# Performance work log

Measured on AMD Instinct MI355X. Metric: run time of the kernel, lower is better.

The kernel has to match this reference:

```python
import jax, jax.numpy as jnp
import numpy as np
from functools import partial

ITERS = 100
EPSILON = 0.8
TAU = 1.02
FEATURE_DIM = 256
MATCHED_THRESHOLD = 0.2
B, D, N0, N1 = 1, 256, 2048, 2048


def log_optimal_transport_extended(scores, alpha, iters, epsilon, tau):
    b, m, n = scores.shape
    dt = scores.dtype
    ms = jnp.asarray(m, dt)
    ns = jnp.asarray(n, dt)
    bins0 = jnp.broadcast_to(alpha, (b, m, 1)).astype(dt)
    bins1 = jnp.broadcast_to(alpha, (b, 1, n)).astype(dt)
    corner = jnp.broadcast_to(alpha, (b, 1, 1)).astype(dt)
    # couplings: [b, m+1, n+1] score matrix augmented with dustbin row/col
    couplings = jnp.concatenate([
        jnp.concatenate([scores, bins0], axis=-1),
        jnp.concatenate([bins1, corner], axis=-1)], axis=1)
    norm = -jnp.log(ms + ns)
    log_mu = jnp.concatenate([jnp.full((m,), norm, dt), (jnp.log(ns) + norm)[None]])
    log_nu = jnp.concatenate([jnp.full((n,), norm, dt), (jnp.log(ms) + norm)[None]])
    log_mu = jnp.broadcast_to(log_mu[None], (b, m + 1))
    log_nu = jnp.broadcast_to(log_nu[None], (b, n + 1))

    def step(carry, _):
        u, v = carry
        u_new = (log_mu - jax.scipy.special.logsumexp(couplings + v[:, None, :], axis=2)) / tau
        u = u + epsilon * (u_new - u)
        v_new = (log_nu - jax.scipy.special.logsumexp(couplings + u[:, :, None], axis=1)) / tau
        v = v + epsilon * (v_new - v)
        return (u, v), None

    u0 = jnp.zeros_like(log_mu)
    v0 = jnp.zeros_like(log_nu)
    (u, v), _ = jax.lax.scan(jax.checkpoint(step), (u0, v0), None, length=iters)
    Z = couplings + u[:, :, None] + v[:, None, :]
    return Z - norm


def reference(mdesc0, mdesc1, bin_score):
    # mdesc0: [b, d, n], mdesc1: [b, d, m]
    sim = jnp.einsum('bdn,bdm->bnm', mdesc0, mdesc1)
    scores = sim / np.float32(np.sqrt(FEATURE_DIM))
    Z = log_optimal_transport_extended(scores, bin_score, ITERS, EPSILON, TAU)
    inner = Z[:, :-1, :-1]                       # [b, m, n]
    m, n = inner.shape[1], inner.shape[2]
    max0_vals = inner.max(axis=2)
    indices0 = inner.argmax(axis=2)              # [b, m] int
    indices1 = inner.argmax(axis=1)              # [b, n] int
    mutual0 = jnp.arange(m)[None, :] == jnp.take_along_axis(indices1, indices0, axis=1)
    mutual1 = jnp.arange(n)[None, :] == jnp.take_along_axis(indices0, indices1, axis=1)
    zero = jnp.zeros((), inner.dtype)
    mscores0 = jnp.where(mutual0, jnp.exp(max0_vals), zero)
    mscores1 = jnp.where(mutual1, jnp.take_along_axis(mscores0, indices1, axis=1), zero)
    valid0 = mutual0 & (mscores0 > MATCHED_THRESHOLD)
    valid1 = mutual1 & jnp.take_along_axis(valid0, indices1, axis=1)
    i0 = jnp.where(valid0, indices0, -1)
    i1 = jnp.where(valid1, indices1, -1)
    return (jnp.exp(Z[0]), i0[0], i1[0], mscores0[0], mscores1[0])


def setup_inputs() -> dict:
    key = jax.random.key(0)
    k0, k1 = jax.random.split(key)
    mdesc0 = jax.random.normal(k0, (B, D, N0), dtype=jnp.float32)
    mdesc1 = jax.random.normal(k1, (B, D, N1), dtype=jnp.float32)
    bin_score = jnp.ones((), dtype=jnp.float32)  # learned dustbin score, init 1.0
    return {"mdesc0": mdesc0, "mdesc1": mdesc1, "bin_score": bin_score}
```

## Files before the change

### kernel.cpp

```cpp
#include <hip/hip_runtime.h>
#include <hip/hip_bf16.h>
#include <math.h>

#define D        256
#define NINNER   2048
#define NROW     2049
#define SP       2064
#define ITERS_N  100
#define EPS_F    0.8f
#define TAU_F    1.02f
#define NB       256
#define NT       256

typedef unsigned long long u64;

#define PSTRIDE  2112u

#define SZ_MAT   (2049u * 2064u)
#define OFF_E    0u
#define OFF_F    SZ_MAT
#define OFF_WUP  (2u * SZ_MAT)
#define OFF_WVP  (OFF_WUP + 4u * PSTRIDE)
#define OFF_MAX0 (OFF_WVP + 4u * PSTRIDE)
#define OFF_IDX0 (OFF_MAX0 + 2048u)
#define OFF_IDX1 (OFF_IDX0 + 2048u)
#define OFF_MS0  (OFF_IDX1 + 2048u)
#define OFF_VLD0 (OFF_MS0 + 2048u)

#define OOFF_Z   0u
#define OOFF_I0  (2049u * 2049u)
#define OOFF_I1  (OOFF_I0 + 2048u)
#define OOFF_S0  (OOFF_I1 + 2048u)
#define OOFF_S1  (OOFF_S0 + 2048u)

__device__ __forceinline__ float    pair_val(u64 x) { return __uint_as_float((unsigned)x); }
__device__ __forceinline__ unsigned pair_tag(u64 x) { return (unsigned)(x >> 32); }
__device__ __forceinline__ u64 make_pair(float v, unsigned t) {
    return ((u64)t << 32) | (u64)__float_as_uint(v);
}

__global__ __launch_bounds__(256) void k_gemm(const float* __restrict__ A,
                                              const float* __restrict__ Bm,
                                              float* __restrict__ E,
                                              float* __restrict__ F) {
    __shared__ float As[8][64];
    __shared__ float Bs[8][64];
    const int tid = threadIdx.x;
    const int tx = tid & 15, ty = tid >> 4;
    const int row0 = blockIdx.y * 64, col0 = blockIdx.x * 64;
    float acc[4][4] = {};
    const int lr = tid >> 6, lc = tid & 63;
    for (int k0 = 0; k0 < D; k0 += 8) {
        As[lr][lc]     = A[(k0 + lr) * NINNER + row0 + lc];
        As[lr + 4][lc] = A[(k0 + lr + 4) * NINNER + row0 + lc];
        Bs[lr][lc]     = Bm[(k0 + lr) * NINNER + col0 + lc];
        Bs[lr + 4][lc] = Bm[(k0 + lr + 4) * NINNER + col0 + lc];
        __syncthreads();
#pragma unroll
        for (int kk = 0; kk < 8; ++kk) {
            const float4 av = *(const float4*)&As[kk][ty * 4];
            const float4 bv = *(const float4*)&Bs[kk][tx * 4];
            const float a_[4] = {av.x, av.y, av.z, av.w};
            const float b_[4] = {bv.x, bv.y, bv.z, bv.w};
#pragma unroll
            for (int r = 0; r < 4; ++r)
#pragma unroll
                for (int c = 0; c < 4; ++c)
                    acc[r][c] = fmaf(a_[r], b_[c], acc[r][c]);
        }
        __syncthreads();
    }
    float o[4][4];
#pragma unroll
    for (int r = 0; r < 4; ++r)
#pragma unroll
        for (int c = 0; c < 4; ++c)
            o[r][c] = expf(acc[r][c] * 0.0625f);
    const int row = row0 + ty * 4, col = col0 + tx * 4;
#pragma unroll
    for (int r = 0; r < 4; ++r)
        *(float4*)(E + (size_t)(row + r) * SP + col)
            = make_float4(o[r][0], o[r][1], o[r][2], o[r][3]);
#pragma unroll
    for (int c = 0; c < 4; ++c)
        *(float4*)(F + (size_t)(col + c) * SP + row)
            = make_float4(o[0][c], o[1][c], o[2][c], o[3][c]);
}

__global__ __launch_bounds__(256) void k_init(float* __restrict__ E,
                                              float* __restrict__ F,
                                              u64* __restrict__ wvb0,
                                              const float* __restrict__ alpha) {
    const int t = blockIdx.x * 256 + threadIdx.x;
    const float ea = expf(alpha[0]);
    if (t < NINNER) {
        E[(size_t)t * SP + NINNER] = ea;
        F[(size_t)t * SP + NINNER] = ea;
    }
    if (t <= NINNER) {
        E[(size_t)NINNER * SP + t] = ea;
        F[(size_t)NINNER * SP + t] = ea;
        wvb0[t] = make_pair(1.0f, 0u);
    }
}

__device__ __forceinline__ void poll8(const u64* buf, int tid, unsigned want, float* w) {
    u64 a[8];
#pragma unroll
    for (int q = 0; q < 8; ++q)
        a[q] = __hip_atomic_load(buf + q * 256 + tid, __ATOMIC_RELAXED, __HIP_MEMORY_SCOPE_AGENT);
    for (;;) {
        unsigned miss = 0u;
#pragma unroll
        for (int q = 0; q < 8; ++q)
            miss |= (pair_tag(a[q]) != want) ? (1u << q) : 0u;
        if (!miss) break;
#pragma unroll
        for (int q = 0; q < 8; ++q)
            if (miss & (1u << q))
                a[q] = __hip_atomic_load(buf + q * 256 + tid, __ATOMIC_RELAXED, __HIP_MEMORY_SCOPE_AGENT);
    }
#pragma unroll
    for (int q = 0; q < 8; ++q) w[q] = pair_val(a[q]);
}

__device__ __forceinline__ float poll_bin(const u64* buf, unsigned want) {
    for (;;) {
        u64 d = __hip_atomic_load(buf + NINNER, __ATOMIC_RELAXED, __HIP_MEMORY_SCOPE_AGENT);
        if (pair_tag(d) == want) return pair_val(d);
    }
}

__global__ __launch_bounds__(256, 1) void k_sinkhorn(const float* __restrict__ E,
                                                     const float* __restrict__ F,
                                                     u64* wub, u64* wvb,
                                                     const float* __restrict__ alpha) {
    const int b = blockIdx.x, tid = threadIdx.x;
    const int lane = tid & 63, wid = tid >> 6;
    const int base = b * 8;
    const bool lastb = (b == NB - 1);
    __shared__ float red[2][4][9];

    const float norm = -8.317766166719343f;
    const float logbin = 7.624618986159398f + norm;
    const float ea = expf(alpha[0]);

    float eR[8][8], fR[8][8];
#pragma unroll
    for (int r = 0; r < 8; ++r) {
        const float* rowE = E + (size_t)(base + r) * SP;
        const float* rowF = F + (size_t)(base + r) * SP;
#pragma unroll
        for (int q = 0; q < 8; ++q) {
            eR[r][q] = rowE[q * 256 + tid];
            fR[r][q] = rowF[q * 256 + tid];
        }
    }

    float u = 0.0f, v = 0.0f;
    float ub = 0.0f, vb = 0.0f;

    for (int it = 0; it < ITERS_N; ++it) {
        {
            u64* src = wvb + (size_t)(it & 1) * PSTRIDE;
            u64* dst = wub + (size_t)((it + 1) & 1) * PSTRIDE;
            const unsigned want = (unsigned)it, prod = (unsigned)(it + 1);
            float w[8];
            poll8(src, tid, want, w);
            const float wd = (tid == 0) ? poll_bin(src, want) : 0.0f;
            float p[8];
#pragma unroll
            for (int r = 0; r < 8; ++r) {
                float s = ea * wd;
#pragma unroll
                for (int q = 0; q < 8; ++q) s = fmaf(eR[r][q], w[q], s);
                p[r] = s;
            }
            float t = w[0] + w[1] + w[2] + w[3] + w[4] + w[5] + w[6] + w[7] + wd;
#pragma unroll
            for (int r = 0; r < 8; ++r) {
                float s = p[r];
#pragma unroll
                for (int m = 1; m < 64; m <<= 1) s += __shfl_xor(s, m, 64);
                if (lane == 0) red[0][wid][r] = s;
            }
#pragma unroll
            for (int m = 1; m < 64; m <<= 1) t += __shfl_xor(t, m, 64);
            if (lane == 0) red[0][wid][8] = t;
            __syncthreads();
            if (tid < 8) {
                const float S = red[0][0][tid] + red[0][1][tid] + red[0][2][tid] + red[0][3][tid];
                const float unew = (norm - logf(S)) / TAU_F;
                u = u + EPS_F * (unew - u);
                __hip_atomic_store(dst + base + tid, make_pair(expf(u), prod),
                                   __ATOMIC_RELAXED, __HIP_MEMORY_SCOPE_AGENT);
            }
            if (lastb && tid == 8) {
                const float S = ea * (red[0][0][8] + red[0][1][8] + red[0][2][8] + red[0][3][8]);
                const float unew = (logbin - logf(S)) / TAU_F;
                ub = ub + EPS_F * (unew - ub);
                __hip_atomic_store(dst + NINNER, make_pair(expf(ub), prod),
                                   __ATOMIC_RELAXED, __HIP_MEMORY_SCOPE_AGENT);
            }
        }
        {
            u64* src = wub + (size_t)((it + 1) & 1) * PSTRIDE;
            u64* dst = wvb + (size_t)((it + 1) & 1) * PSTRIDE;
            const unsigned want = (unsigned)(it + 1), prod = (unsigned)(it + 1);
            float w[8];
            poll8(src, tid, want, w);
            const float wd = (tid == 0) ? poll_bin(src, want) : 0.0f;
            float p[8];
#pragma unroll
            for (int r = 0; r < 8; ++r) {
                float s = ea * wd;
#pragma unroll
                for (int q = 0; q < 8; ++q) s = fmaf(fR[r][q], w[q], s);
                p[r] = s;
            }
            float t = w[0] + w[1] + w[2] + w[3] + w[4] + w[5] + w[6] + w[7] + wd;
#pragma unroll
            for (int r = 0; r < 8; ++r) {
                float s = p[r];
#pragma unroll
                for (int m = 1; m < 64; m <<= 1) s += __shfl_xor(s, m, 64);
                if (lane == 0) red[1][wid][r] = s;
            }
#pragma unroll
            for (int m = 1; m < 64; m <<= 1) t += __shfl_xor(t, m, 64);
            if (lane == 0) red[1][wid][8] = t;
            __syncthreads();
            if (tid < 8) {
                const float T = red[1][0][tid] + red[1][1][tid] + red[1][2][tid] + red[1][3][tid];
                const float vnew = (norm - logf(T)) / TAU_F;
                v = v + EPS_F * (vnew - v);
                __hip_atomic_store(dst + base + tid, make_pair(expf(v), prod),
                                   __ATOMIC_RELAXED, __HIP_MEMORY_SCOPE_AGENT);
            }
            if (lastb && tid == 8) {
                const float T = ea * (red[1][0][8] + red[1][1][8] + red[1][2][8] + red[1][3][8]);
                const float vnew = (logbin - logf(T)) / TAU_F;
                vb = vb + EPS_F * (vnew - vb);
                __hip_atomic_store(dst + NINNER, make_pair(expf(vb), prod),
                                   __ATOMIC_RELAXED, __HIP_MEMORY_SCOPE_AGENT);
            }
        }
    }
}

__global__ __launch_bounds__(256) void k_finish(const float* __restrict__ E,
                                                const float* __restrict__ F,
                                                const float2* __restrict__ wup,
                                                const float2* __restrict__ wvp,
                                                float* __restrict__ out,
                                                float* __restrict__ max0,
                                                int* __restrict__ idx0,
                                                int* __restrict__ idx1) {
    const int i = blockIdx.x;
    const int tid = threadIdx.x;
    const int lane = tid & 63, wid = tid >> 6;
    __shared__ float sb[4]; __shared__ int si[4];

    {
        const float wui = wup[i].x * 4096.0f;
        const float* row = E + (size_t)i * SP;
        float best = -1.0f; int bidx = 0;
        for (int j = tid; j < NROW; j += 256) {
            const float val = row[j] * wvp[j].x * wui;
            out[(size_t)i * NROW + j] = val;
            if (j < NINNER && val > best) { best = val; bidx = j; }
        }
        if (i < NINNER) {
#pragma unroll
            for (int m = 1; m < 64; m <<= 1) {
                const float ob = __shfl_xor(best, m, 64);
                const int   oi = __shfl_xor(bidx, m, 64);
                if (ob > best || (ob == best && oi < bidx)) { best = ob; bidx = oi; }
            }
            if (lane == 0) { sb[wid] = best; si[wid] = bidx; }
            __syncthreads();
            if (tid == 0) {
                for (int k = 1; k < 4; ++k)
                    if (sb[k] > best || (sb[k] == best && si[k] < bidx)) { best = sb[k]; bidx = si[k]; }
                max0[i] = best; idx0[i] = bidx;
            }
        }
    }

    if (i < NINNER) {
        __syncthreads();
        const float* row = F + (size_t)i * SP;
        float best = -1.0f; int bidx = 0;
        for (int r = tid; r < NINNER; r += 256) {
            const float q = row[r] * wup[r].x;
            if (q > best) { best = q; bidx = r; }
        }
#pragma unroll
        for (int m = 1; m < 64; m <<= 1) {
            const float ob = __shfl_xor(best, m, 64);
            const int   oi = __shfl_xor(bidx, m, 64);
            if (ob > best || (ob == best && oi < bidx)) { best = ob; bidx = oi; }
        }
        if (lane == 0) { sb[wid] = best; si[wid] = bidx; }
        __syncthreads();
        if (tid == 0) {
            for (int k = 1; k < 4; ++k)
                if (sb[k] > best || (sb[k] == best && si[k] < bidx)) { best = sb[k]; bidx = si[k]; }
            idx1[i] = bidx;
        }
    }
}

__global__ __launch_bounds__(256) void k_match0(const float* __restrict__ max0,
                                                const int* __restrict__ idx0,
                                                const int* __restrict__ idx1,
                                                float* __restrict__ ms0,
                                                int* __restrict__ vld0,
                                                float* __restrict__ out) {
    const int i = blockIdx.x * 256 + threadIdx.x;
    if (i >= NINNER) return;
    const int j = idx0[i];
    const bool mut = (idx1[j] == i);
    const float ms = mut ? max0[i] : 0.0f;
    const bool val = mut && (ms > 0.2f);
    ms0[i] = ms; vld0[i] = val ? 1 : 0;
    out[OOFF_I0 + i] = val ? (float)j : -1.0f;
    out[OOFF_S0 + i] = ms;
}
__global__ __launch_bounds__(256) void k_match1(const int* __restrict__ idx0,
                                                const int* __restrict__ idx1,
                                                const float* __restrict__ ms0,
                                                const int* __restrict__ vld0,
                                                float* __restrict__ out) {
    const int j = blockIdx.x * 256 + threadIdx.x;
    if (j >= NINNER) return;
    const int i = idx1[j];
    const bool mut = (idx0[i] == j);
    const float ms = mut ? ms0[i] : 0.0f;
    const bool val = mut && (vld0[i] != 0);
    out[OOFF_I1 + j] = val ? (float)i : -1.0f;
    out[OOFF_S1 + j] = ms;
}

extern "C" void kernel_launch(void* const* d_in, const int* in_sizes, int n_in,
                              void* d_out, int out_size, void* d_ws, size_t ws_size,
                              hipStream_t stream) {
    const float* A     = (const float*)d_in[0];
    const float* Bm    = (const float*)d_in[1];
    const float* alpha = (const float*)d_in[2];

    float* ws = (float*)d_ws;
    float* E    = ws + OFF_E;
    float* F    = ws + OFF_F;
    u64*   wub  = (u64*)(ws + OFF_WUP);
    u64*   wvb  = (u64*)(ws + OFF_WVP);
    float* max0 = ws + OFF_MAX0;
    int*   idx0 = (int*)(ws + OFF_IDX0);
    int*   idx1 = (int*)(ws + OFF_IDX1);
    float* ms0  = ws + OFF_MS0;
    int*   vld0 = (int*)(ws + OFF_VLD0);
    float* out  = (float*)d_out;

    k_gemm<<<dim3(32, 32), 256, 0, stream>>>(A, Bm, E, F);
    k_init<<<dim3(16), 256, 0, stream>>>(E, F, wvb, alpha);
    k_sinkhorn<<<dim3(NB), NT, 0, stream>>>(E, F, wub, wvb, alpha);
    k_finish<<<dim3(NROW), 256, 0, stream>>>(E, F, (const float2*)wub, (const float2*)wvb,
                                             out, max0, idx0, idx1);
    k_match0<<<dim3(8), 256, 0, stream>>>(max0, idx0, idx1, ms0, vld0, out);
    k_match1<<<dim3(8), 256, 0, stream>>>(idx0, idx1, ms0, vld0, out);
}
```

Before: 918.7 us.

## Compute dustbin scalars redundantly per block instead of polling shared bin entry

Each block now computes the dustbin row and column potentials locally from the block-reduced column sum and its own copy of the other bin potential. This removes the serialized poll on the single bin slot that every block previously waited on each half-iteration. The final bin values are published once after the loop. It also adds an s_sleep backoff in the polling loop to reduce memory contention, which may add some wake-up latency.

```diff
diff --git a/kernel.cpp b/kernel.cpp
--- a/kernel.cpp
+++ b/kernel.cpp
@@ -96,11 +96,11 @@
     if (t < NINNER) {
         E[(size_t)t * SP + NINNER] = ea;
         F[(size_t)t * SP + NINNER] = ea;
+        wvb0[t] = make_pair(1.0f, 0u);
     }
     if (t <= NINNER) {
         E[(size_t)NINNER * SP + t] = ea;
         F[(size_t)NINNER * SP + t] = ea;
-        wvb0[t] = make_pair(1.0f, 0u);
     }
 }
 
@@ -115,6 +115,7 @@
         for (int q = 0; q < 8; ++q)
             miss |= (pair_tag(a[q]) != want) ? (1u << q) : 0u;
         if (!miss) break;
+        __builtin_amdgcn_s_sleep(2);
 #pragma unroll
         for (int q = 0; q < 8; ++q)
             if (miss & (1u << q))
@@ -122,13 +123,6 @@
     }
 #pragma unroll
     for (int q = 0; q < 8; ++q) w[q] = pair_val(a[q]);
-}
-
-__device__ __forceinline__ float poll_bin(const u64* buf, unsigned want) {
-    for (;;) {
-        u64 d = __hip_atomic_load(buf + NINNER, __ATOMIC_RELAXED, __HIP_MEMORY_SCOPE_AGENT);
-        if (pair_tag(d) == want) return pair_val(d);
-    }
 }
 
 __global__ __launch_bounds__(256, 1) void k_sinkhorn(const float* __restrict__ E,
@@ -159,24 +153,24 @@
 
     float u = 0.0f, v = 0.0f;
     float ub = 0.0f, vb = 0.0f;
+    float eub = 1.0f, evb = 1.0f;
 
     for (int it = 0; it < ITERS_N; ++it) {
         {
-            u64* src = wvb + (size_t)(it & 1) * PSTRIDE;
+            const u64* src = wvb + (size_t)(it & 1) * PSTRIDE;
             u64* dst = wub + (size_t)((it + 1) & 1) * PSTRIDE;
-            const unsigned want = (unsigned)it, prod = (unsigned)(it + 1);
+            const unsigned prod = (unsigned)(it + 1);
             float w[8];
-            poll8(src, tid, want, w);
-            const float wd = (tid == 0) ? poll_bin(src, want) : 0.0f;
+            poll8(src, tid, (unsigned)it, w);
             float p[8];
 #pragma unroll
             for (int r = 0; r < 8; ++r) {
-                float s = ea * wd;
+                float s = 0.0f;
 #pragma unroll
                 for (int q = 0; q < 8; ++q) s = fmaf(eR[r][q], w[q], s);
                 p[r] = s;
             }
-            float t = w[0] + w[1] + w[2] + w[3] + w[4] + w[5] + w[6] + w[7] + wd;
+            float t = w[0] + w[1] + w[2] + w[3] + w[4] + w[5] + w[6] + w[7];
 #pragma unroll
             for (int r = 0; r < 8; ++r) {
                 float s = p[r];
@@ -188,37 +182,34 @@
             for (int m = 1; m < 64; m <<= 1) t += __shfl_xor(t, m, 64);
             if (lane == 0) red[0][wid][8] = t;
             __syncthreads();
+            const float tsum = red[0][0][8] + red[0][1][8] + red[0][2][8] + red[0][3][8];
+            const float Sbin = ea * (tsum + evb);
+            ub = ub + EPS_F * ((logbin - logf(Sbin)) / TAU_F - ub);
             if (tid < 8) {
-                const float S = red[0][0][tid] + red[0][1][tid] + red[0][2][tid] + red[0][3][tid];
+                const float S = red[0][0][tid] + red[0][1][tid] + red[0][2][tid] + red[0][3][tid]
+                              + ea * evb;
                 const float unew = (norm - logf(S)) / TAU_F;
                 u = u + EPS_F * (unew - u);
                 __hip_atomic_store(dst + base + tid, make_pair(expf(u), prod),
                                    __ATOMIC_RELAXED, __HIP_MEMORY_SCOPE_AGENT);
             }
-            if (lastb && tid == 8) {
-                const float S = ea * (red[0][0][8] + red[0][1][8] + red[0][2][8] + red[0][3][8]);
-                const float unew = (logbin - logf(S)) / TAU_F;
-                ub = ub + EPS_F * (unew - ub);
-                __hip_atomic_store(dst + NINNER, make_pair(expf(ub), prod),
-                                   __ATOMIC_RELAXED, __HIP_MEMORY_SCOPE_AGENT);
-            }
+            eub = expf(ub);
         }
         {
-            u64* src = wub + (size_t)((it + 1) & 1) * PSTRIDE;
+            const u64* src = wub + (size_t)((it + 1) & 1) * PSTRIDE;
             u64* dst = wvb + (size_t)((it + 1) & 1) * PSTRIDE;
-            const unsigned want = (unsigned)(it + 1), prod = (unsigned)(it + 1);
+            const unsigned prod = (unsigned)(it + 1);
             float w[8];
-            poll8(src, tid, want, w);
-            const float wd = (tid == 0) ? poll_bin(src, want) : 0.0f;
+            poll8(src, tid, prod, w);
             float p[8];
 #pragma unroll
             for (int r = 0; r < 8; ++r) {
-                float s = ea * wd;
+                float s = 0.0f;
 #pragma unroll
                 for (int q = 0; q < 8; ++q) s = fmaf(fR[r][q], w[q], s);
                 p[r] = s;
             }
-            float t = w[0] + w[1] + w[2] + w[3] + w[4] + w[5] + w[6] + w[7] + wd;
+            float t = w[0] + w[1] + w[2] + w[3] + w[4] + w[5] + w[6] + w[7];
 #pragma unroll
             for (int r = 0; r < 8; ++r) {
                 float s = p[r];
@@ -230,21 +221,25 @@
             for (int m = 1; m < 64; m <<= 1) t += __shfl_xor(t, m, 64);
             if (lane == 0) red[1][wid][8] = t;
             __syncthreads();
+            const float tsum = red[1][0][8] + red[1][1][8] + red[1][2][8] + red[1][3][8];
+            const float Tbin = ea * (tsum + eub);
+            vb = vb + EPS_F * ((logbin - logf(Tbin)) / TAU_F - vb);
             if (tid < 8) {
-                const float T = red[1][0][tid] + red[1][1][tid] + red[1][2][tid] + red[1][3][tid];
+                const float T = red[1][0][tid] + red[1][1][tid] + red[1][2][tid] + red[1][3][tid]
+                              + ea * eub;
                 const float vnew = (norm - logf(T)) / TAU_F;
                 v = v + EPS_F * (vnew - v);
                 __hip_atomic_store(dst + base + tid, make_pair(expf(v), prod),
                                    __ATOMIC_RELAXED, __HIP_MEMORY_SCOPE_AGENT);
             }
-            if (lastb && tid == 8) {
-                const float T = ea * (red[1][0][8] + red[1][1][8] + red[1][2][8] + red[1][3][8]);
-                const float vnew = (logbin - logf(T)) / TAU_F;
-                vb = vb + EPS_F * (vnew - vb);
-                __hip_atomic_store(dst + NINNER, make_pair(expf(vb), prod),
-                                   __ATOMIC_RELAXED, __HIP_MEMORY_SCOPE_AGENT);
-            }
-        }
+            evb = expf(vb);
+        }
+    }
+    if (lastb && tid == 0) {
+        __hip_atomic_store(wub + NINNER, make_pair(eub, (unsigned)ITERS_N),
+                           __ATOMIC_RELAXED, __HIP_MEMORY_SCOPE_AGENT);
+        __hip_atomic_store(wvb + NINNER, make_pair(evb, (unsigned)ITERS_N),
+                           __ATOMIC_RELAXED, __HIP_MEMORY_SCOPE_AGENT);
     }
 }
 
```

Result: faster. 899.7 us (-2.1%).
